# Kernel tuning notes

Hardware: AMD Instinct MI355X
Metric: run time of the kernel (lower is better)

## Reference

```python
import jax, jax.numpy as jnp
import numpy as np

B, T, C = 2, 2048, 2048
H, HK = 16, 4
HD = C // H
N_REP = H // HK


def setup_inputs() -> dict:
    key = jax.random.key(0)
    ks = jax.random.split(key, 10)
    sc_in = 1.0 / np.sqrt(C)
    x = jax.random.normal(ks[0], (B, T, C), dtype=jnp.float32)
    # rotary embeddings (realistic cos/sin from inv_freq)
    inv_freq = 1.0 / (10000.0 ** (jnp.arange(0, HD, 2, dtype=jnp.float32) / HD))
    freqs = jnp.arange(T, dtype=jnp.float32)[:, None] * inv_freq[None, :]  # [T, HD/2]
    emb = jnp.concatenate([freqs, freqs], axis=-1)  # [T, HD]
    cos = jnp.broadcast_to(jnp.cos(emb)[None], (B, T, HD))
    sin = jnp.broadcast_to(jnp.sin(emb)[None], (B, T, HD))
    Wq = jax.random.normal(ks[1], (C, H * HD), dtype=jnp.float32) * sc_in
    bq = jnp.zeros((H * HD,), dtype=jnp.float32)
    Wk = jax.random.normal(ks[2], (C, HK * HD), dtype=jnp.float32) * sc_in
    bk = jnp.zeros((HK * HD,), dtype=jnp.float32)
    Wv = jax.random.normal(ks[3], (C, HK * HD), dtype=jnp.float32) * sc_in
    bv = jnp.zeros((HK * HD,), dtype=jnp.float32)
    Wo = jax.random.normal(ks[4], (C, C), dtype=jnp.float32) * sc_in
    return {"x": x, "cos": cos, "sin": sin, "Wq": Wq, "bq": bq,
            "Wk": Wk, "bk": bk, "Wv": Wv, "bv": bv, "Wo": Wo}


def _rotate_half(t):
    t1, t2 = jnp.split(t, 2, axis=-1)
    return jnp.concatenate([-t2, t1], axis=-1)


def reference(x, cos, sin, Wq, bq, Wk, bk, Wv, bv, Wo):
    b, t, c = x.shape
    q = (x @ Wq + bq).reshape(b, t, H, HD).transpose(0, 2, 1, 3)   # [B,H,T,HD]
    k = (x @ Wk + bk).reshape(b, t, HK, HD).transpose(0, 2, 1, 3)  # [B,HK,T,HD]
    v = (x @ Wv + bv).reshape(b, t, HK, HD).transpose(0, 2, 1, 3)  # [B,HK,T,HD]
    co = cos[:, None, :, :]  # [B,1,T,HD]
    si = sin[:, None, :, :]
    q = q * co + _rotate_half(q) * si
    k = k * co + _rotate_half(k) * si
    # GQA without materializing repeated K/V: group query heads per KV head
    qg = q.reshape(b, HK, N_REP, t, HD)
    scale = 1.0 / np.sqrt(HD)
    scores = jnp.einsum('bgrqd,bgkd->bgrqk', qg, k) * scale  # [B,HK,n_rep,T,T]
    causal = jnp.tril(jnp.ones((t, t), dtype=bool))
    scores = jnp.where(causal, scores, jnp.finfo(scores.dtype).min)
    att = jax.nn.softmax(scores, axis=-1)
    yg = jnp.einsum('bgrqk,bgkd->bgrqd', att, v)  # [B,HK,n_rep,T,HD]
    y = yg.reshape(b, H, t, HD).transpose(0, 2, 1, 3).reshape(b, t, c)
    return y @ Wo
```

## Files before the change

### kernel.cpp

```cpp
#include <hip/hip_runtime.h>
#include <math.h>

#define BB 2
#define TT 2048
#define CC 2048
#define HH 16
#define HKK 4
#define HD 128
#define MM (BB*TT)

typedef short bf16x8 __attribute__((ext_vector_type(8)));
typedef float f32x4 __attribute__((ext_vector_type(4)));
typedef float f32x16 __attribute__((ext_vector_type(16)));
typedef int   i32x4 __attribute__((ext_vector_type(4)));

#define GLOBAL_AS(p) ((const __attribute__((address_space(1))) void*)(p))
#define LDS_AS(p)    ((__attribute__((address_space(3))) void*)(p))

__device__ __forceinline__ unsigned short f2bf(float f) {
    unsigned u = __float_as_uint(f);
    u += 0x7fff + ((u >> 16) & 1);
    return (unsigned short)(u >> 16);
}
__device__ __forceinline__ float bf2f(unsigned short h) {
    return __uint_as_float(((unsigned)h) << 16);
}

#define QSCALE (0.08838834764831845f * 1.44269504088896340736f)

__global__ __launch_bounds__(256) void cast_x_kernel(
    const float* __restrict__ x, unsigned short* __restrict__ xb)
{
    size_t i = ((size_t)blockIdx.x * 256 + threadIdx.x) * 8;
    float4 a = *(const float4*)&x[i];
    float4 b = *(const float4*)&x[i + 4];
    uint4 r;
    r.x = f2bf(a.x) | ((unsigned)f2bf(a.y) << 16);
    r.y = f2bf(a.z) | ((unsigned)f2bf(a.w) << 16);
    r.z = f2bf(b.x) | ((unsigned)f2bf(b.y) << 16);
    r.w = f2bf(b.z) | ((unsigned)f2bf(b.w) << 16);
    *(uint4*)&xb[i] = r;
}

__global__ __launch_bounds__(256) void wtrans_kernel(
    const float* __restrict__ Wq, const float* __restrict__ Wk,
    const float* __restrict__ Wv, const float* __restrict__ Wo,
    unsigned short* __restrict__ Wt, unsigned short* __restrict__ Wot)
{
    __shared__ float tile[64][65];
    int z = blockIdx.z;
    const float* src; unsigned short* dst; int ldW, nmax, noff;
    if (z == 0)      { src = Wq; dst = Wt;  ldW = 2048; nmax = 2048; noff = 0; }
    else if (z == 1) { src = Wk; dst = Wt;  ldW = 512;  nmax = 512;  noff = 2048; }
    else if (z == 2) { src = Wv; dst = Wt;  ldW = 512;  nmax = 512;  noff = 2560; }
    else             { src = Wo; dst = Wot; ldW = 2048; nmax = 2048; noff = 0; }
    int n0 = blockIdx.y * 64;
    if (n0 >= nmax) return;
    int k0 = blockIdx.x * 64;
    int tx = threadIdx.x & 15, ty = threadIdx.x >> 4;
#pragma unroll
    for (int i = 0; i < 4; ++i) {
        int r = ty + i * 16;
        float4 v4 = *(const float4*)&src[(size_t)(k0 + r) * ldW + n0 + tx * 4];
        tile[r][tx * 4 + 0] = v4.x;
        tile[r][tx * 4 + 1] = v4.y;
        tile[r][tx * 4 + 2] = v4.z;
        tile[r][tx * 4 + 3] = v4.w;
    }
    __syncthreads();
#pragma unroll
    for (int i = 0; i < 4; ++i) {
        int r = ty + i * 16;
        int c = tx * 4;
        ushort4 o;
        o.x = f2bf(tile[c + 0][r]);
        o.y = f2bf(tile[c + 1][r]);
        o.z = f2bf(tile[c + 2][r]);
        o.w = f2bf(tile[c + 3][r]);
        *(ushort4*)&dst[(size_t)(noff + n0 + r) * 2048 + k0 + c] = o;
    }
}

__device__ __forceinline__ void gemm_core_128x128x64(
    const unsigned short* __restrict__ A, const unsigned short* __restrict__ B,
    short* As, short* Bs, int m0, int n0,
    const int* mrow, const int* nrow, f32x4 (&acc)[4][4])
{
    const int tid = threadIdx.x;
    const int lane = tid & 63;
    const int w = tid >> 6;
    const int lm = lane & 15;
    const int q8 = lane >> 4;
    const int lrow = lane >> 3;
    const int lchunk = lane & 7;

    for (int kt = 0; kt < CC; kt += 64) {
        __syncthreads();
#pragma unroll
        for (int jj = 0; jj < 4; ++jj) {
            int rA = w * 32 + jj * 8 + lrow;
            int cA = ((lchunk ^ (rA & 7)) << 3);
            __builtin_amdgcn_global_load_lds(
                GLOBAL_AS(&A[(size_t)(m0 + rA) * CC + kt + cA]),
                LDS_AS(&As[(w * 32 + jj * 8) * 64]), 16, 0, 0);
            __builtin_amdgcn_global_load_lds(
                GLOBAL_AS(&B[(size_t)(n0 + rA) * CC + kt + cA]),
                LDS_AS(&Bs[(w * 32 + jj * 8) * 64]), 16, 0, 0);
        }
        __syncthreads();
#pragma unroll
        for (int ksi = 0; ksi < 2; ++ksi) {
            bf16x8 af[4], bfr[4];
#pragma unroll
            for (int i = 0; i < 4; ++i) {
                int xo = (((ksi * 4 + q8) ^ (lm & 7)) << 3);
                af[i]  = *(const bf16x8*)&As[(mrow[i] + lm) * 64 + xo];
                bfr[i] = *(const bf16x8*)&Bs[(nrow[i] + lm) * 64 + xo];
            }
#pragma unroll
            for (int im = 0; im < 4; ++im)
#pragma unroll
                for (int in = 0; in < 4; ++in)
                    acc[im][in] = __builtin_amdgcn_mfma_f32_16x16x32_bf16(af[im], bfr[in], acc[im][in], 0, 0, 0);
        }
    }
}

__global__ __launch_bounds__(256, 3) void qkv_gemm_mfma(
    const unsigned short* __restrict__ xb, const unsigned short* __restrict__ Wt,
    const float* __restrict__ bq, const float* __restrict__ bk, const float* __restrict__ bv,
    const float* __restrict__ cosb, const float* __restrict__ sinb,
    unsigned short* __restrict__ q, unsigned short* __restrict__ k, unsigned short* __restrict__ v)
{
    __shared__ __attribute__((aligned(16))) short As[128 * 64];
    __shared__ __attribute__((aligned(16))) short Bs[128 * 64];
    const int lane = threadIdx.x & 63;
    const int w = threadIdx.x >> 6;
    const int w1 = w >> 1;
    const int m0 = blockIdx.y * 128;
    const int n0 = blockIdx.x * 128;
    const int lm = lane & 15;
    const int q8 = lane >> 4;

    int mrow[4], nrow[4];
#pragma unroll
    for (int i = 0; i < 4; ++i) {
        mrow[i] = (w & 1) * 64 + i * 16;
        nrow[i] = w1 * 32 + (i & 1) * 16 + (i >> 1) * 64;
    }

    f32x4 acc[4][4];
#pragma unroll
    for (int im = 0; im < 4; ++im)
#pragma unroll
        for (int in = 0; in < 4; ++in) acc[im][in] = {0.f, 0.f, 0.f, 0.f};

    gemm_core_128x128x64(xb, Wt, As, Bs, m0, n0, mrow, nrow, acc);

    unsigned short* dst; const float* bias; int ldD, off, mode;
    if (n0 < 2048)      { dst = q; bias = bq; ldD = 2048; off = n0;        mode = 0; }
    else if (n0 < 2560) { dst = k; bias = bk; ldD = 512;  off = n0 - 2048; mode = 1; }
    else                { dst = v; bias = bv; ldD = 512;  off = n0 - 2560; mode = 2; }

    float bv_[4];
#pragma unroll
    for (int in = 0; in < 4; ++in) bv_[in] = bias[off + nrow[in] + lm];

#pragma unroll
    for (int im = 0; im < 4; ++im) {
        int rowbase = m0 + mrow[im] + q8 * 4;
        float t[4][4];
#pragma unroll
        for (int in = 0; in < 4; ++in)
#pragma unroll
            for (int r = 0; r < 4; ++r) t[in][r] = acc[im][in][r] + bv_[in];
        if (mode < 2) {
#pragma unroll
            for (int in = 0; in < 4; ++in) {
                int d = nrow[in] + lm;
                float sgn = (in < 2) ? -1.f : 1.f;
#pragma unroll
                for (int r = 0; r < 4; ++r) {
                    int row = rowbase + r;
                    float c = cosb[row * HD + d];
                    float s = sinb[row * HD + d];
                    float o = c * t[in][r] + sgn * s * t[in ^ 2][r];
                    if (mode == 0) o *= QSCALE;
                    dst[(size_t)row * ldD + off + d] = f2bf(o);
                }
            }
        } else {
#pragma unroll
            for (int in = 0; in < 4; ++in)
#pragma unroll
                for (int r = 0; r < 4; ++r)
                    dst[(size_t)(rowbase + r) * ldD + off + nrow[in] + lm] = f2bf(t[in][r]);
        }
    }
}

__global__ __launch_bounds__(256, 3) void out_gemm_mfma(
    const unsigned short* __restrict__ yb, const unsigned short* __restrict__ Wot,
    float* __restrict__ Cout)
{
    __shared__ __attribute__((aligned(16))) short As[128 * 64];
    __shared__ __attribute__((aligned(16))) short Bs[128 * 64];
    const int lane = threadIdx.x & 63;
    const int w = threadIdx.x >> 6;
    const int m0 = blockIdx.y * 128;
    const int n0 = blockIdx.x * 128;
    const int lm = lane & 15;
    const int q8 = lane >> 4;

    int mrow[4], nrow[4];
#pragma unroll
    for (int i = 0; i < 4; ++i) {
        mrow[i] = (w & 1) * 64 + i * 16;
        nrow[i] = (w >> 1) * 64 + i * 16;
    }

    f32x4 acc[4][4];
#pragma unroll
    for (int im = 0; im < 4; ++im)
#pragma unroll
        for (int in = 0; in < 4; ++in) acc[im][in] = {0.f, 0.f, 0.f, 0.f};

    gemm_core_128x128x64(yb, Wot, As, Bs, m0, n0, mrow, nrow, acc);

#pragma unroll
    for (int im = 0; im < 4; ++im)
#pragma unroll
        for (int in = 0; in < 4; ++in)
#pragma unroll
            for (int r = 0; r < 4; ++r) {
                int row = m0 + mrow[im] + q8 * 4 + r;
                Cout[(size_t)row * CC + n0 + nrow[in] + lm] = acc[im][in][r];
            }
}

__global__ __launch_bounds__(256) void vtrans_kernel(
    const unsigned short* __restrict__ v, unsigned short* __restrict__ vt)
{
    __shared__ unsigned short tile[64][68];
    int bg = blockIdx.z;
    int b = bg >> 2, g = bg & 3;
    int t0 = blockIdx.x * 64;
    int d0 = blockIdx.y * 64;
    int tx = threadIdx.x & 15, ty = threadIdx.x >> 4;
#pragma unroll
    for (int i = 0; i < 4; ++i) {
        int r = ty + i * 16;
        ushort4 v4 = *(const ushort4*)&v[(size_t)(b * TT + t0 + r) * (HKK * HD) + g * HD + d0 + tx * 4];
        tile[r][tx * 4 + 0] = v4.x;
        tile[r][tx * 4 + 1] = v4.y;
        tile[r][tx * 4 + 2] = v4.z;
        tile[r][tx * 4 + 3] = v4.w;
    }
    __syncthreads();
#pragma unroll
    for (int i = 0; i < 4; ++i) {
        int r = ty + i * 16;
        int c = tx * 4;
        ushort4 o;
        o.x = tile[c + 0][r];
        o.y = tile[c + 1][r];
        o.z = tile[c + 2][r];
        o.w = tile[c + 3][r];
        *(ushort4*)&vt[(size_t)(bg * HD + d0 + r) * TT + t0 + c] = o;
    }
}

static __device__ const signed char QI_T[24] = {
    15, 7, 14, 14, 13, 6, 12, 11,
    15, 13, 12, 10, 10, 9, 11, 5,
    0, 1, 2, 3, 8, 4, 8, 9
};
static __device__ const signed char HF_T[24] = {
    0, 2, 0, 1, 1, 2, 1, 1,
    1, 0, 0, 0, 1, 0, 0, 2,
    2, 2, 2, 2, 0, 2, 1, 1
};

__global__ __launch_bounds__(256, 2) void flash_mfma(
    const unsigned short* __restrict__ q, const unsigned short* __restrict__ k,
    const unsigned short* __restrict__ vt, unsigned short* __restrict__ y,
    float* __restrict__ po, float* __restrict__ sb)
{
    __shared__ __attribute__((aligned(16))) short SM[32768];

    const int tid = threadIdx.x;
    const int lane = tid & 63;
    const int w = tid >> 6;
    const int l31 = lane & 31;
    const int hi = lane >> 5;
    const int swz = (l31 & 7) << 3;
    const int bh = blockIdx.x;
    const int b = bh >> 4, h = bh & 15, g = h >> 2;
    const int yb_ = blockIdx.y;
    const int qi = QI_T[yb_];
    const int hf = HF_T[yb_];
    const int q0 = qi * 128;
    const int jdiag = 2 * qi + (w >> 1);
    int j0, jend;
    if (hf == 2)      { j0 = 0;      jend = 2 * qi + 2; }
    else if (hf == 0) { j0 = 0;      jend = qi + 1; }
    else              { j0 = qi + 1; jend = 2 * qi + 2; }

    bf16x8 qf[8];
#pragma unroll
    for (int ks = 0; ks < 8; ++ks)
        qf[ks] = *(const bf16x8*)&q[(size_t)(b * TT + q0 + w * 32 + l31) * CC
                                    + h * HD + ks * 16 + hi * 8];

    f32x16 o_acc[4];
#pragma unroll
    for (int t = 0; t < 4; ++t)
#pragma unroll
        for (int e = 0; e < 16; ++e) o_acc[t][e] = 0.f;
    float m_i = -1e30f;
    float l_i = 0.f;

    const unsigned short* kbase = k + (size_t)(b * TT) * (HKK * HD) + g * HD;
    const unsigned short* vbase = vt + (size_t)((b * 4 + g) * HD) * TT;
    int ko[4], vo[4];
#pragma unroll
    for (int i = 0; i < 4; ++i) {
        int c = (i * 4 + w) * 64 + lane;
        int kt_ = c >> 4, kc = c & 15;
        ko[i] = kt_ * (HKK * HD) + ((kc ^ (kt_ & 7)) << 3);
        int dv = c >> 3, vc = c & 7;
        vo[i] = dv * TT + ((vc ^ (dv & 7)) << 3);
    }

#define STAGE(cb, jj) do {                                                   \
    short* Kd = SM + (cb) * 16384;                                           \
    short* Vd = Kd + 8192;                                                   \
    _Pragma("unroll")                                                        \
    for (int i_ = 0; i_ < 4; ++i_) {                                         \
        int blk_ = (i_ * 4 + w) * 512;                                       \
        __builtin_amdgcn_global_load_lds(                                    \
            GLOBAL_AS(kbase + (size_t)(jj) * 64 * (HKK * HD) + ko[i_]),      \
            LDS_AS(Kd + blk_), 16, 0, 0);                                    \
        __builtin_amdgcn_global_load_lds(                                    \
            GLOBAL_AS(vbase + (size_t)(jj) * 64 + vo[i_]),                   \
            LDS_AS(Vd + blk_), 16, 0, 0);                                    \
    }                                                                        \
} while (0)

    STAGE(0, j0);
    __syncthreads();

    int c = 0;
    for (int j = j0; j < jend; ++j) {
        if (j + 1 < jend) STAGE(c ^ 1, j + 1);

        if (j <= jdiag) {
            const short* Ks = SM + c * 16384;
            const short* Vs = Ks + 8192;
            f32x16 sacc[2];
#pragma unroll
            for (int ct = 0; ct < 2; ++ct) {
#pragma unroll
                for (int e = 0; e < 16; ++e) sacc[ct][e] = 0.f;
#pragma unroll
                for (int ks = 0; ks < 8; ++ks) {
                    bf16x8 kf = *(const bf16x8*)&Ks[(ct * 32 + l31) * 128
                                                    + (((2 * ks + hi) << 3) ^ swz)];
                    sacc[ct] = __builtin_amdgcn_mfma_f32_32x32x16_bf16(kf, qf[ks], sacc[ct], 0, 0, 0);
                }
            }
            if (j == jdiag) {
                int lim = l31 + 32 * (w & 1);
#pragma unroll
                for (int ct = 0; ct < 2; ++ct)
#pragma unroll
                    for (int reg = 0; reg < 16; ++reg) {
                        int tok = ct * 32 + (reg & 3) + 8 * (reg >> 2) + 4 * hi;
                        if (tok > lim) sacc[ct][reg] = -1e30f;
                    }
            }
            float mx[8];
#pragma unroll
            for (int e = 0; e < 8; ++e)
                mx[e] = fmaxf(fmaxf(sacc[0][e], sacc[0][e + 8]),
                              fmaxf(sacc[1][e], sacc[1][e + 8]));
            float tmax = fmaxf(fmaxf(fmaxf(mx[0], mx[1]), fmaxf(mx[2], mx[3])),
                               fmaxf(fmaxf(mx[4], mx[5]), fmaxf(mx[6], mx[7])));
            tmax = fmaxf(tmax, __shfl_xor(tmax, 32));
            float m_new = fmaxf(m_i, tmax);
            float alpha = exp2f(m_i - m_new);
            m_i = m_new;

#pragma unroll
            for (int ct = 0; ct < 2; ++ct)
#pragma unroll
                for (int e = 0; e < 16; ++e)
                    sacc[ct][e] = exp2f(sacc[ct][e] - m_new);
            float s8[8];
#pragma unroll
            for (int e = 0; e < 8; ++e)
                s8[e] = (sacc[0][e] + sacc[0][e + 8]) + (sacc[1][e] + sacc[1][e + 8]);
            float ps = ((s8[0] + s8[1]) + (s8[2] + s8[3]))
                     + ((s8[4] + s8[5]) + (s8[6] + s8[7]));
            l_i = l_i * alpha + ps;

#pragma unroll
            for (int t = 0; t < 4; ++t)
#pragma unroll
                for (int e = 0; e < 16; ++e) o_acc[t][e] *= alpha;

            int W[2][4][2];
#pragma unroll
            for (int ct = 0; ct < 2; ++ct)
#pragma unroll
                for (int bb = 0; bb < 4; ++bb)
#pragma unroll
                    for (int jj2 = 0; jj2 < 2; ++jj2)
                        asm("v_cvt_pk_bf16_f32 %0, %1, %2"
                            : "=v"(W[ct][bb][jj2])
                            : "v"(sacc[ct][4 * bb + 2 * jj2]), "v"(sacc[ct][4 * bb + 2 * jj2 + 1]));

#pragma unroll
            for (int ks = 0; ks < 4; ++ks) {
                int a0 = W[ks >> 1][2 * (ks & 1)][0];
                int a1 = W[ks >> 1][2 * (ks & 1)][1];
                int b0 = W[ks >> 1][2 * (ks & 1) + 1][0];
                int b1 = W[ks >> 1][2 * (ks & 1) + 1][1];
                asm("v_permlane32_swap_b32 %0, %1" : "+v"(a0), "+v"(b0));
                asm("v_permlane32_swap_b32 %0, %1" : "+v"(a1), "+v"(b1));
                i32x4 wv; wv[0] = a0; wv[1] = a1; wv[2] = b0; wv[3] = b1;
                bf16x8 pa = __builtin_bit_cast(bf16x8, wv);
#pragma unroll
                for (int t = 0; t < 4; ++t) {
                    bf16x8 vf = *(const bf16x8*)&Vs[(t * 32 + l31) * 64
                                                    + (((2 * ks + hi) << 3) ^ swz)];
                    o_acc[t] = __builtin_amdgcn_mfma_f32_32x32x16_bf16(vf, pa, o_acc[t], 0, 0, 0);
                }
            }
        }

        __syncthreads();
        c ^= 1;
    }
#undef STAGE

    float lf = l_i + __shfl_xor(l_i, 32);
    float invl = 1.f / lf;

    if (hf == 2) {
        short* Es = SM;
#pragma unroll
        for (int t = 0; t < 4; ++t)
#pragma unroll
            for (int rg = 0; rg < 4; ++rg) {
                ushort4 o;
                o.x = f2bf(o_acc[t][rg * 4 + 0] * invl);
                o.y = f2bf(o_acc[t][rg * 4 + 1] * invl);
                o.z = f2bf(o_acc[t][rg * 4 + 2] * invl);
                o.w = f2bf(o_acc[t][rg * 4 + 3] * invl);
                *(ushort4*)&Es[(w * 32 + l31) * 136 + t * 32 + 8 * rg + 4 * hi] = o;
            }
        __syncthreads();
#pragma unroll
        for (int i = 0; i < 8; ++i) {
            int f = tid + i * 256;
            int row = f >> 4, ch = f & 15;
            uint4 tv = *(const uint4*)&Es[row * 136 + ch * 8];
            *(uint4*)&y[(size_t)(b * TT + q0 + row) * CC + h * HD + ch * 8] = tv;
        }
    } else {
        const int pi = ((bh << 3) + (qi - 8)) * 2 + hf;
        if (hi == 0) sb[pi * 128 + w * 32 + l31] = lf * exp2f(m_i);
        float* pb = po + (size_t)pi * 16384;
#pragma unroll
        for (int t = 0; t < 4; ++t)
#pragma unroll
            for (int rg = 0; rg < 4; ++rg) {
                float4 o;
                o.x = o_acc[t][rg * 4 + 0] * invl;
                o.y = o_acc[t][rg * 4 + 1] * invl;
                o.z = o_acc[t][rg * 4 + 2] * invl;
                o.w = o_acc[t][rg * 4 + 3] * invl;
                *(float4*)&pb[(w * 32 + l31) * 128 + t * 32 + 8 * rg + 4 * hi] = o;
            }
    }
}

__global__ __launch_bounds__(256) void combine_kernel(
    const float* __restrict__ po, const float* __restrict__ sb,
    unsigned short* __restrict__ y)
{
    const int bh = blockIdx.x;
    const int b = bh >> 4, h = bh & 15;
    const int qi = 8 + blockIdx.y;
    const int p0 = ((bh << 3) + (qi - 8)) * 2;
    const int t = threadIdx.x;
    const int row = t >> 1, d0 = (t & 1) * 64;
    float s0 = sb[p0 * 128 + row];
    float s1 = sb[(p0 + 1) * 128 + row];
    float w0 = s0 / (s0 + s1);
    float w1 = 1.f - w0;
    const float* a = &po[(size_t)p0 * 16384 + row * 128 + d0];
    const float* c = &po[(size_t)(p0 + 1) * 16384 + row * 128 + d0];
    unsigned short* yr = &y[(size_t)(b * TT + qi * 128 + row) * CC + h * HD + d0];
#pragma unroll
    for (int i = 0; i < 64; i += 4) {
        float4 xa = *(const float4*)&a[i];
        float4 xc = *(const float4*)&c[i];
        ushort4 o;
        o.x = f2bf(w0 * xa.x + w1 * xc.x);
        o.y = f2bf(w0 * xa.y + w1 * xc.y);
        o.z = f2bf(w0 * xa.z + w1 * xc.z);
        o.w = f2bf(w0 * xa.w + w1 * xc.w);
        *(ushort4*)&yr[i] = o;
    }
}

extern "C" void kernel_launch(void* const* d_in, const int* in_sizes, int n_in,
                              void* d_out, int out_size, void* d_ws, size_t ws_size,
                              hipStream_t stream) {
    const float* x    = (const float*)d_in[0];
    const float* cosb = (const float*)d_in[1];
    const float* sinb = (const float*)d_in[2];
    const float* Wq   = (const float*)d_in[3];
    const float* bq   = (const float*)d_in[4];
    const float* Wk   = (const float*)d_in[5];
    const float* bk   = (const float*)d_in[6];
    const float* Wv   = (const float*)d_in[7];
    const float* bv   = (const float*)d_in[8];
    const float* Wo   = (const float*)d_in[9];
    float* out = (float*)d_out;

    unsigned short* xb  = (unsigned short*)d_ws;
    unsigned short* Wt  = xb  + (size_t)MM * CC;
    unsigned short* Wot = Wt  + (size_t)3072 * 2048;
    unsigned short* qb  = Wot + (size_t)2048 * 2048;
    unsigned short* kb  = qb  + (size_t)MM * CC;
    unsigned short* vb  = kb  + (size_t)MM * (HKK * HD);
    unsigned short* vtb = vb  + (size_t)MM * (HKK * HD);
    unsigned short* ybf = vtb + (size_t)BB * HKK * HD * TT;

    float* po = (float*)d_out;
    float* sbuf = (float*)xb;

    cast_x_kernel<<<dim3((MM * CC) / 2048), 256, 0, stream>>>(x, xb);
    wtrans_kernel<<<dim3(32, 32, 4), 256, 0, stream>>>(Wq, Wk, Wv, Wo, Wt, Wot);
    qkv_gemm_mfma<<<dim3(3072 / 128, MM / 128), 256, 0, stream>>>(
        xb, Wt, bq, bk, bv, cosb, sinb, qb, kb, vb);
    vtrans_kernel<<<dim3(TT / 64, HD / 64, BB * HKK), 256, 0, stream>>>(vb, vtb);
    flash_mfma<<<dim3(BB * HH, 24), 256, 0, stream>>>(qb, kb, vtb, ybf, po, sbuf);
    combine_kernel<<<dim3(BB * HH, 8), 256, 0, stream>>>(po, sbuf, ybf);
    out_gemm_mfma<<<dim3(CC / 128, MM / 128), 256, 0, stream>>>(ybf, Wot, out);
}
```

Before: 318.0 us.

## Single-buffer V in flash attention, raise occupancy, and merge prep kernels

The flash kernel now double-buffers only K and single-buffers V in LDS. That cuts shared memory from 64KB to 48KB so launch bounds can allow 3 blocks per CU. V for the current tile is loaded at the start of each iteration and waited for, via vmcnt and a barrier, after the QK/softmax phase, which overlaps the V load with score compute. The bf16 packing of P moves to after the barrier, and the x-cast and weight-transpose kernels are merged into one launch. Risks include the extra barrier per iteration, register pressure at the higher occupancy, and a redundant K load on the last iteration.

```diff
diff --git a/kernel.cpp b/kernel.cpp
--- a/kernel.cpp
+++ b/kernel.cpp
@@ -28,27 +28,27 @@
 
 #define QSCALE (0.08838834764831845f * 1.44269504088896340736f)
 
-__global__ __launch_bounds__(256) void cast_x_kernel(
-    const float* __restrict__ x, unsigned short* __restrict__ xb)
-{
-    size_t i = ((size_t)blockIdx.x * 256 + threadIdx.x) * 8;
-    float4 a = *(const float4*)&x[i];
-    float4 b = *(const float4*)&x[i + 4];
-    uint4 r;
-    r.x = f2bf(a.x) | ((unsigned)f2bf(a.y) << 16);
-    r.y = f2bf(a.z) | ((unsigned)f2bf(a.w) << 16);
-    r.z = f2bf(b.x) | ((unsigned)f2bf(b.y) << 16);
-    r.w = f2bf(b.z) | ((unsigned)f2bf(b.w) << 16);
-    *(uint4*)&xb[i] = r;
-}
-
-__global__ __launch_bounds__(256) void wtrans_kernel(
-    const float* __restrict__ Wq, const float* __restrict__ Wk,
-    const float* __restrict__ Wv, const float* __restrict__ Wo,
+__global__ __launch_bounds__(256) void prep_kernel(
+    const float* __restrict__ x, const float* __restrict__ Wq,
+    const float* __restrict__ Wk, const float* __restrict__ Wv,
+    const float* __restrict__ Wo, unsigned short* __restrict__ xb,
     unsigned short* __restrict__ Wt, unsigned short* __restrict__ Wot)
 {
     __shared__ float tile[64][65];
     int z = blockIdx.z;
+    if (z >= 4) {
+        int bid = (z - 4) * 1024 + blockIdx.y * 32 + blockIdx.x;
+        size_t i = ((size_t)bid * 256 + threadIdx.x) * 8;
+        float4 a = *(const float4*)&x[i];
+        float4 b = *(const float4*)&x[i + 4];
+        uint4 r;
+        r.x = f2bf(a.x) | ((unsigned)f2bf(a.y) << 16);
+        r.y = f2bf(a.z) | ((unsigned)f2bf(a.w) << 16);
+        r.z = f2bf(b.x) | ((unsigned)f2bf(b.y) << 16);
+        r.w = f2bf(b.z) | ((unsigned)f2bf(b.w) << 16);
+        *(uint4*)&xb[i] = r;
+        return;
+    }
     const float* src; unsigned short* dst; int ldW, nmax, noff;
     if (z == 0)      { src = Wq; dst = Wt;  ldW = 2048; nmax = 2048; noff = 0; }
     else if (z == 1) { src = Wk; dst = Wt;  ldW = 512;  nmax = 512;  noff = 2048; }
@@ -281,12 +281,13 @@
     2, 2, 2, 2, 0, 2, 1, 1
 };
 
-__global__ __launch_bounds__(256, 2) void flash_mfma(
+__global__ __launch_bounds__(256, 3) void flash_mfma(
     const unsigned short* __restrict__ q, const unsigned short* __restrict__ k,
     const unsigned short* __restrict__ vt, unsigned short* __restrict__ y,
     float* __restrict__ po, float* __restrict__ sb)
 {
-    __shared__ __attribute__((aligned(16))) short SM[32768];
+    __shared__ __attribute__((aligned(16))) short SM[24576];
+    short* Vs = SM + 16384;
 
     const int tid = threadIdx.x;
     const int lane = tid & 63;
@@ -332,32 +333,34 @@
         vo[i] = dv * TT + ((vc ^ (dv & 7)) << 3);
     }
 
-#define STAGE(cb, jj) do {                                                   \
-    short* Kd = SM + (cb) * 16384;                                           \
-    short* Vd = Kd + 8192;                                                   \
+#define STAGE_K(cb, jj) do {                                                 \
+    short* Kd = SM + (cb) * 8192;                                            \
     _Pragma("unroll")                                                        \
-    for (int i_ = 0; i_ < 4; ++i_) {                                         \
-        int blk_ = (i_ * 4 + w) * 512;                                       \
+    for (int i_ = 0; i_ < 4; ++i_)                                           \
         __builtin_amdgcn_global_load_lds(                                    \
             GLOBAL_AS(kbase + (size_t)(jj) * 64 * (HKK * HD) + ko[i_]),      \
-            LDS_AS(Kd + blk_), 16, 0, 0);                                    \
+            LDS_AS(Kd + (i_ * 4 + w) * 512), 16, 0, 0);                      \
+} while (0)
+#define STAGE_V(jj) do {                                                     \
+    _Pragma("unroll")                                                        \
+    for (int i_ = 0; i_ < 4; ++i_)                                           \
         __builtin_amdgcn_global_load_lds(                                    \
             GLOBAL_AS(vbase + (size_t)(jj) * 64 + vo[i_]),                   \
-            LDS_AS(Vd + blk_), 16, 0, 0);                                    \
-    }                                                                        \
+            LDS_AS(Vs + (i_ * 4 + w) * 512), 16, 0, 0);                      \
 } while (0)
 
-    STAGE(0, j0);
+    STAGE_K(0, j0);
     __syncthreads();
 
     int c = 0;
     for (int j = j0; j < jend; ++j) {
-        if (j + 1 < jend) STAGE(c ^ 1, j + 1);
-
+        STAGE_V(j);
+        int jn = (j + 1 < jend) ? j + 1 : j;
+        STAGE_K(c ^ 1, jn);
+
+        f32x16 sacc[2];
         if (j <= jdiag) {
-            const short* Ks = SM + c * 16384;
-            const short* Vs = Ks + 8192;
-            f32x16 sacc[2];
+            const short* Ks = SM + c * 8192;
 #pragma unroll
             for (int ct = 0; ct < 2; ++ct) {
 #pragma unroll
@@ -408,24 +411,26 @@
             for (int t = 0; t < 4; ++t)
 #pragma unroll
                 for (int e = 0; e < 16; ++e) o_acc[t][e] *= alpha;
-
-            int W[2][4][2];
-#pragma unroll
-            for (int ct = 0; ct < 2; ++ct)
-#pragma unroll
-                for (int bb = 0; bb < 4; ++bb)
-#pragma unroll
-                    for (int jj2 = 0; jj2 < 2; ++jj2)
-                        asm("v_cvt_pk_bf16_f32 %0, %1, %2"
-                            : "=v"(W[ct][bb][jj2])
-                            : "v"(sacc[ct][4 * bb + 2 * jj2]), "v"(sacc[ct][4 * bb + 2 * jj2 + 1]));
-
+        }
+
+        asm volatile("s_waitcnt vmcnt(4)" ::: "memory");
+        __builtin_amdgcn_sched_barrier(0);
+        __builtin_amdgcn_s_barrier();
+        __builtin_amdgcn_sched_barrier(0);
+
+        if (j <= jdiag) {
 #pragma unroll
             for (int ks = 0; ks < 4; ++ks) {
-                int a0 = W[ks >> 1][2 * (ks & 1)][0];
-                int a1 = W[ks >> 1][2 * (ks & 1)][1];
-                int b0 = W[ks >> 1][2 * (ks & 1) + 1][0];
-                int b1 = W[ks >> 1][2 * (ks & 1) + 1][1];
+                const int ct = ks >> 1, base = 8 * (ks & 1);
+                int a0, a1, b0, b1;
+                asm("v_cvt_pk_bf16_f32 %0, %1, %2" : "=v"(a0)
+                    : "v"(sacc[ct][base + 0]), "v"(sacc[ct][base + 1]));
+                asm("v_cvt_pk_bf16_f32 %0, %1, %2" : "=v"(a1)
+                    : "v"(sacc[ct][base + 2]), "v"(sacc[ct][base + 3]));
+                asm("v_cvt_pk_bf16_f32 %0, %1, %2" : "=v"(b0)
+                    : "v"(sacc[ct][base + 4]), "v"(sacc[ct][base + 5]));
+                asm("v_cvt_pk_bf16_f32 %0, %1, %2" : "=v"(b1)
+                    : "v"(sacc[ct][base + 6]), "v"(sacc[ct][base + 7]));
                 asm("v_permlane32_swap_b32 %0, %1" : "+v"(a0), "+v"(b0));
                 asm("v_permlane32_swap_b32 %0, %1" : "+v"(a1), "+v"(b1));
                 i32x4 wv; wv[0] = a0; wv[1] = a1; wv[2] = b0; wv[3] = b1;
@@ -442,7 +447,8 @@
         __syncthreads();
         c ^= 1;
     }
-#undef STAGE
+#undef STAGE_K
+#undef STAGE_V
 
     float lf = l_i + __shfl_xor(l_i, 32);
     float invl = 1.f / lf;
@@ -543,8 +549,7 @@
     float* po = (float*)d_out;
     float* sbuf = (float*)xb;
 
-    cast_x_kernel<<<dim3((MM * CC) / 2048), 256, 0, stream>>>(x, xb);
-    wtrans_kernel<<<dim3(32, 32, 4), 256, 0, stream>>>(Wq, Wk, Wv, Wo, Wt, Wot);
+    prep_kernel<<<dim3(32, 32, 8), 256, 0, stream>>>(x, Wq, Wk, Wv, Wo, xb, Wt, Wot);
     qkv_gemm_mfma<<<dim3(3072 / 128, MM / 128), 256, 0, stream>>>(
         xb, Wt, bq, bk, bv, cosb, sinb, qb, kb, vb);
     vtrans_kernel<<<dim3(TT / 64, HD / 64, BB * HKK), 256, 0, stream>>>(vb, vtb);
```

After: 312.7 us. Within noise of the previous version (-1.7%).
